# Optimization experiments

Hardware: AMD Instinct MI355X
Metric: run time of the kernel (lower is better)

## Reference

```python
import jax, jax.numpy as jnp
import numpy as np

B, S, DIN, DOUT, H = 4, 2048, 512, 512, 8
DH = DOUT // H
EPS = 1e-5


def _conv_bn(x, conv_w, conv_b, bn_gamma, bn_beta, bn_mean, bn_var):
    # x: [B, S, DIN] -> permute to [B, DIN, S] like torch
    xc = jnp.transpose(x, (0, 2, 1))
    y = jax.lax.conv_general_dilated(
        xc, conv_w, window_strides=(1,), padding=[(3, 3)],
        dimension_numbers=('NCH', 'OIH', 'NCH'))  # [B, DOUT, S]
    y = y + conv_b[None, :, None]
    # BatchNorm1d in eval mode: normalize per channel with running stats
    inv = jax.lax.rsqrt(bn_var + EPS)
    y = (y - bn_mean[None, :, None]) * (inv * bn_gamma)[None, :, None] + bn_beta[None, :, None]
    return jnp.transpose(y, (0, 2, 1))  # back to [B, S, DOUT]


def setup_inputs() -> dict:
    key = jax.random.key(0)
    ks = jax.random.split(key, 4)
    return {
        'q': jax.random.normal(ks[0], (B, S, DIN), dtype=jnp.float32),
        'k': jax.random.normal(ks[1], (B, S, DIN), dtype=jnp.float32),
        'v': jax.random.normal(ks[2], (B, S, DIN), dtype=jnp.float32),
        'conv_w': jax.random.normal(ks[3], (DOUT, DIN, 7), dtype=jnp.float32) * 0.02,
        'conv_b': jnp.zeros((DOUT,), jnp.float32),
        'bn_gamma': jnp.ones((DOUT,), jnp.float32),
        'bn_beta': jnp.zeros((DOUT,), jnp.float32),
        'bn_mean': jnp.zeros((DOUT,), jnp.float32),
        'bn_var': jnp.ones((DOUT,), jnp.float32),
        'ln_gamma': jnp.ones((DOUT,), jnp.float32),
        'ln_beta': jnp.zeros((DOUT,), jnp.float32),
    }


def reference(q, k, v, conv_w, conv_b, bn_gamma, bn_beta, bn_mean, bn_var,
              ln_gamma, ln_beta):
    # shared conv+BN preproc applied to q, k, v, then split into heads [B,S,H,DH]
    qh = _conv_bn(q, conv_w, conv_b, bn_gamma, bn_beta, bn_mean, bn_var).reshape(B, S, H, DH)
    kh = _conv_bn(k, conv_w, conv_b, bn_gamma, bn_beta, bn_mean, bn_var).reshape(B, S, H, DH)
    vh = _conv_bn(v, conv_w, conv_b, bn_gamma, bn_beta, bn_mean, bn_var).reshape(B, S, H, DH)
    # full QK^T score matrix, scaled, softmax, times V (mask is None)
    scores = jnp.einsum('bqhd,bkhd->bhqk', qh, kh) * (1.0 / np.sqrt(DH).astype(np.float32))
    probs = jax.nn.softmax(scores, axis=-1)
    out = jnp.einsum('bhqk,bkhd->bqhd', probs, vh).reshape(B, S, DOUT)
    # dropout(p=0) is identity; final LayerNorm over feature dim
    mu = jnp.mean(out, axis=-1, keepdims=True)
    var = jnp.mean(jnp.square(out - mu), axis=-1, keepdims=True)
    return (out - mu) * jax.lax.rsqrt(var + EPS) * ln_gamma + ln_beta
```

## Files before the change

### kernel.cpp

```cpp
#include <hip/hip_runtime.h>
#include <hip/hip_bf16.h>


#define B_ 4
#define S_ 2048
#define DIN_ 512
#define DOUT_ 512
#define H_ 8
#define DH_ 64
#define EPS_ 1e-5f
#define SP_ 2054

using bf16x8 = __attribute__((ext_vector_type(8))) short;
using f32x4  = __attribute__((ext_vector_type(4))) float;

__device__ __forceinline__ unsigned short f2bf(float x) {
    union { float f; unsigned u; } v; v.f = x;
    unsigned r = v.u + 0x7FFF + ((v.u >> 16) & 1);
    return (unsigned short)(r >> 16);
}

__device__ __forceinline__ unsigned cvt2(float lo, float hi) {
    unsigned r;
    asm("v_cvt_pk_bf16_f32 %0, %1, %2" : "=v"(r) : "v"(lo), "v"(hi));
    return r;
}

typedef __attribute__((address_space(1))) const unsigned int GU32;
typedef __attribute__((address_space(3))) unsigned int LU32;
__device__ __forceinline__ void gl_lds16(const void* g, void* l) {
    __builtin_amdgcn_global_load_lds((GU32*)g, (LU32*)l, 16, 0, 0);
}

__global__ void cast_x(const float* __restrict__ q, const float* __restrict__ k,
                       const float* __restrict__ v, unsigned short* __restrict__ xb) {
    int i = blockIdx.x * 256 + threadIdx.x;
    int row = i >> 6;
    int cin = (i & 63) * 8;
    int tb = row / SP_;
    int pr = row - tb * SP_;
    int tensor = tb >> 2;
    int b = tb & 3;
    unsigned short* dst = xb + (size_t)row * DIN_ + cin;
    if (pr < 3 || pr >= SP_ - 3) {
        *reinterpret_cast<uint4*>(dst) = make_uint4(0, 0, 0, 0);
    } else {
        const float* src = (tensor == 0 ? q : (tensor == 1 ? k : v)) +
                           ((size_t)b * S_ + (pr - 3)) * DIN_ + cin;
        float4 a0 = *reinterpret_cast<const float4*>(src);
        float4 a1 = *reinterpret_cast<const float4*>(src + 4);
        uint4 o;
        o.x = cvt2(a0.x, a0.y); o.y = cvt2(a0.z, a0.w);
        o.z = cvt2(a1.x, a1.y); o.w = cvt2(a1.z, a1.w);
        *reinterpret_cast<uint4*>(dst) = o;
    }
}

__global__ void prep_w(const float* __restrict__ w, const float* __restrict__ cb,
                       const float* __restrict__ gamma, const float* __restrict__ beta,
                       const float* __restrict__ mean, const float* __restrict__ var,
                       unsigned short* __restrict__ w_eff, float* __restrict__ b_eff) {
    int gid = blockIdx.x * blockDim.x + threadIdx.x;
    if (gid < DOUT_) {
        float sc = gamma[gid] * rsqrtf(var[gid] + EPS_);
        b_eff[gid] = (cb[gid] - mean[gid]) * sc + beta[gid];
    }
    int total = 7 * DOUT_ * DIN_;
    for (int i = gid; i < total; i += gridDim.x * blockDim.x) {
        int t = i / (DOUT_ * DIN_);
        int rem = i - t * (DOUT_ * DIN_);
        int co = rem >> 9;
        int ci = rem & 511;
        float sc = gamma[co] * rsqrtf(var[co] + EPS_);
        w_eff[i] = f2bf(w[(co * DIN_ + ci) * 7 + t] * sc);
    }
}

__global__ __launch_bounds__(256, 2) void conv_bn(
        const unsigned short* __restrict__ xb,
        const unsigned short* __restrict__ w_eff,
        const float* __restrict__ b_eff,
        unsigned short* __restrict__ out3) {
    __shared__ alignas(16) unsigned short As[2][192 * 32];
    __shared__ alignas(16) unsigned short Bs[3][256 * 32];

    int orig = blockIdx.x;
    int bid = (orig & 7) * 48 + (orig >> 3);
    int tensor = bid >> 7;
    int rem = bid & 127;
    int batch = rem >> 5;
    int stile = (rem >> 1) & 15;
    int cotile = rem & 1;
    int s0 = stile * 128;
    int co0 = cotile * 256;

    const unsigned short* xp = xb + (size_t)(tensor * 4 + batch) * SP_ * DIN_;
    unsigned short* out = out3 + (size_t)tensor * (B_ * S_ * DOUT_) +
                          (size_t)batch * S_ * DOUT_;

    const int tid = threadIdx.x;
    const int l = tid & 63;
    const int wv = tid >> 6;
    const int g = l >> 4;
    const int c16 = l & 15;
    const int wrow = (wv >> 1) * 64;
    const int wcol = (wv & 1) * 128;

    const int dr4 = l >> 2;
    const int sch = ((l & 3) ^ (dr4 & 3)) << 3;

#define STAGE_A(cc, buf) do {                                                   \
        _Pragma("unroll")                                                       \
        for (int j = 0; j < 3; ++j) {                                           \
            int r0 = (wv * 3 + j) * 16;                                         \
            int rs = r0 + dr4; if (rs > 133) rs = 133;                          \
            gl_lds16(xp + (size_t)(s0 + rs) * DIN_ + (cc) * 32 + sch,           \
                     &As[buf][r0 * 32]);                                        \
        }                                                                       \
    } while (0)

#define STAGE_B(cc, t, buf) do {                                                \
        const unsigned short* wp = w_eff + (size_t)(t) * (DOUT_ * DIN_) +       \
                                   (cc) * 32;                                   \
        _Pragma("unroll")                                                       \
        for (int j = 0; j < 4; ++j) {                                           \
            int r0 = (wv * 4 + j) * 16;                                         \
            gl_lds16(wp + (size_t)(co0 + r0 + dr4) * DIN_ + sch,                \
                     &Bs[buf][r0 * 32]);                                        \
        }                                                                       \
    } while (0)

    f32x4 acc[4][8] = {};

    STAGE_A(0, 0);
    STAGE_B(0, 0, 0);
    int bcur = 0;

    for (int cc = 0; cc < 16; ++cc) {
        const int ca = cc & 1;
        for (int t = 0; t < 7; ++t) {
            int bnext = bcur + 1; if (bnext == 3) bnext = 0;
            if (t < 6) {
                STAGE_B(cc, t + 1, bnext);
                asm volatile("s_waitcnt vmcnt(4)" ::: "memory");
            } else if (cc < 15) {
                STAGE_B(cc + 1, 0, bnext);
                STAGE_A(cc + 1, ca ^ 1);
                asm volatile("s_waitcnt vmcnt(7)" ::: "memory");
            } else {
                asm volatile("s_waitcnt vmcnt(0)" ::: "memory");
            }
            __builtin_amdgcn_s_barrier();

            const unsigned short* Ab = &As[ca][0];
            const unsigned short* Bb = &Bs[bcur][0];
            bf16x8 af[4], bfv[8];
#pragma unroll
            for (int m = 0; m < 4; ++m) {
                int r = wrow + m * 16 + c16 + t;
                af[m] = *reinterpret_cast<const bf16x8*>(
                    &Ab[r * 32 + ((g ^ (r & 3)) << 3)]);
            }
#pragma unroll
            for (int n = 0; n < 8; ++n) {
                int rb = wcol + n * 16 + c16;
                bfv[n] = *reinterpret_cast<const bf16x8*>(
                    &Bb[rb * 32 + ((g ^ (rb & 3)) << 3)]);
            }
            __builtin_amdgcn_s_setprio(1);
#pragma unroll
            for (int m = 0; m < 4; ++m)
#pragma unroll
                for (int n = 0; n < 8; ++n)
                    acc[m][n] = __builtin_amdgcn_mfma_f32_16x16x32_bf16(
                        af[m], bfv[n], acc[m][n], 0, 0, 0);
            __builtin_amdgcn_s_setprio(0);
            bcur = bnext;
        }
    }

    float osc = (tensor == 0) ? 0.125f : 1.0f;
#pragma unroll
    for (int m = 0; m < 4; ++m) {
        int rowb = s0 + wrow + m * 16 + 4 * g;
#pragma unroll
        for (int n = 0; n < 8; ++n) {
            int col = co0 + wcol + n * 16 + c16;
            float be = b_eff[col];
#pragma unroll
            for (int ri = 0; ri < 4; ++ri)
                out[(size_t)(rowb + ri) * DOUT_ + col] =
                    f2bf((acc[m][n][ri] + be) * osc);
        }
    }
#undef STAGE_A
#undef STAGE_B
}

__global__ void transpose_v(const unsigned short* __restrict__ vh,
                            unsigned short* __restrict__ vt) {
    __shared__ alignas(16) unsigned short T[64 * 64];
    int bid = blockIdx.x;
    int stile = bid & 31;
    int bh = bid >> 5;
    int b = bh >> 3;
    int h = bh & 7;
    int s0 = stile * 64;
    const unsigned short* src = vh + ((size_t)b * S_ + s0) * DOUT_ + h * DH_;
    unsigned short* dst = vt + (size_t)bh * DH_ * S_ + s0;
    int tid = threadIdx.x;
#pragma unroll
    for (int it = 0; it < 2; ++it) {
        int idx = tid + it * 256;
        int s = idx >> 3, dhc = idx & 7;
        uint4 val = *reinterpret_cast<const uint4*>(&src[(size_t)s * DOUT_ + dhc * 8]);
        *reinterpret_cast<uint4*>(&T[s * 64 + ((dhc ^ (s & 7) ^ ((s >> 3) & 7)) << 3)]) = val;
    }
    __syncthreads();
#pragma unroll
    for (int it = 0; it < 2; ++it) {
        int idx = tid + it * 256;
        int dh = idx >> 3, sc = idx & 7;
        unsigned short tmp[8];
#pragma unroll
        for (int j = 0; j < 8; ++j) {
            int s = sc * 8 + j;
            tmp[j] = T[s * 64 + (((dh >> 3) ^ (s & 7) ^ ((s >> 3) & 7)) << 3) + (dh & 7)];
        }
        *reinterpret_cast<uint4*>(&dst[(size_t)dh * S_ + sc * 8]) =
            *reinterpret_cast<const uint4*>(tmp);
    }
}

__global__ __launch_bounds__(256, 4) void attn(const unsigned short* __restrict__ qh,
                     const unsigned short* __restrict__ kh,
                     const unsigned short* __restrict__ vt,
                     float* __restrict__ out) {
    __shared__ alignas(16) unsigned short Ks[2][64 * 64];
    __shared__ alignas(16) unsigned short Vs[2][64 * 64];
    __shared__ alignas(16) unsigned short Ps[4][16 * 64];

    const int tid = threadIdx.x;
    const int l = tid & 63;
    const int wv = tid >> 6;
    const int g = l >> 4;
    const int c16 = l & 15;

    const int orig = blockIdx.x;
    const int bid = ((orig & 7) << 7) + (orig >> 3);
    const int qt = bid & 31;
    const int bh = bid >> 5;
    const int b = bh >> 3;
    const int h = bh & 7;
    const int s0 = qt * 64;

    const unsigned short* qp = qh + (size_t)b * S_ * DOUT_ + h * DH_;
    const unsigned short* kp = kh + (size_t)b * S_ * DOUT_ + h * DH_;
    const unsigned short* vp = vt + (size_t)bh * DH_ * S_;

    bf16x8 qf[2];
    {
        int row = s0 + wv * 16 + c16;
        qf[0] = *reinterpret_cast<const bf16x8*>(&qp[(size_t)row * DOUT_ + 8 * g]);
        qf[1] = *reinterpret_cast<const bf16x8*>(&qp[(size_t)row * DOUT_ + 32 + 8 * g]);
    }

    const int l3 = l >> 3;
    const int kchunk8 = ((l & 7) ^ l3) * 8;

#define STAGE(kt, buf) do {                                                          \
        const unsigned short* kgp = kp + (size_t)(kt) * 64 * DOUT_;                  \
        const unsigned short* vgp = vp + (size_t)(kt) * 64;                          \
        _Pragma("unroll")                                                            \
        for (int i = 0; i < 2; ++i) {                                                \
            int K0 = wv * 16 + i * 8;                                                \
            gl_lds16(kgp + (size_t)(K0 + l3) * DOUT_ + kchunk8, &Ks[buf][K0 * 64]);  \
            gl_lds16(vgp + (size_t)(K0 + l3) * S_   + kchunk8, &Vs[buf][K0 * 64]);   \
        }                                                                            \
    } while (0)

    f32x4 oacc[4] = {};
    float mrow[4], lrow[4];
#pragma unroll
    for (int r = 0; r < 4; ++r) { mrow[r] = -1e30f; lrow[r] = 0.f; }

    char* PsB = (char*)&Ps[wv][0];

    STAGE(0, 0);

    const int NT = S_ / 64;
    for (int kt = 0; kt < NT; ++kt) {
        const int cur = kt & 1;
        if (kt + 1 < NT) {
            STAGE(kt + 1, 1 - cur);
            asm volatile("s_waitcnt vmcnt(4)" ::: "memory");
        } else {
            asm volatile("s_waitcnt vmcnt(0)" ::: "memory");
        }
        __builtin_amdgcn_s_barrier();

        const char* KsB = (const char*)&Ks[cur][0];
        f32x4 sf[4] = {};
#pragma unroll
        for (int kk = 0; kk < 2; ++kk) {
            bf16x8 kf[4];
#pragma unroll
            for (int n = 0; n < 4; ++n)
                kf[n] = *reinterpret_cast<const bf16x8*>(
                    KsB + (n * 16 + c16) * 128 + (((4 * kk + g) ^ (l & 7)) << 4));
            __builtin_amdgcn_s_setprio(1);
#pragma unroll
            for (int n = 0; n < 4; ++n)
                sf[n] = __builtin_amdgcn_mfma_f32_16x16x32_bf16(qf[kk], kf[n], sf[n], 0, 0, 0);
            __builtin_amdgcn_s_setprio(0);
        }

        float mnew[4], corr[4];
#pragma unroll
        for (int r = 0; r < 4; ++r) {
            float mx = fmaxf(fmaxf(sf[0][r], sf[1][r]), fmaxf(sf[2][r], sf[3][r]));
            mx = fmaxf(mx, __shfl_xor(mx, 1, 64));
            mx = fmaxf(mx, __shfl_xor(mx, 2, 64));
            mx = fmaxf(mx, __shfl_xor(mx, 4, 64));
            mx = fmaxf(mx, __shfl_xor(mx, 8, 64));
            mnew[r] = fmaxf(mrow[r], mx);
            corr[r] = __expf(mrow[r] - mnew[r]);
            mrow[r] = mnew[r];
        }
        float rs[4] = {0.f, 0.f, 0.f, 0.f};
#pragma unroll
        for (int n = 0; n < 4; ++n)
#pragma unroll
            for (int r = 0; r < 4; ++r) {
                float p = __expf(sf[n][r] - mnew[r]);
                sf[n][r] = p;
                rs[r] += p;
            }
#pragma unroll
        for (int r = 0; r < 4; ++r) {
            rs[r] += __shfl_xor(rs[r], 1, 64);
            rs[r] += __shfl_xor(rs[r], 2, 64);
            rs[r] += __shfl_xor(rs[r], 4, 64);
            rs[r] += __shfl_xor(rs[r], 8, 64);
            lrow[r] = lrow[r] * corr[r] + rs[r];
            oacc[0][r] *= corr[r];
            oacc[1][r] *= corr[r];
            oacc[2][r] *= corr[r];
            oacc[3][r] *= corr[r];
        }

#pragma unroll
        for (int n = 0; n < 4; ++n) {
            int cb = 2 * n + (c16 >> 3);
#pragma unroll
            for (int r = 0; r < 4; ++r) {
                int row = 4 * g + r;
                int phys = cb ^ (row & 7) ^ (row >> 3);
                *(unsigned short*)(PsB + row * 128 + (phys << 4) + ((l & 7) << 1)) =
                    f2bf(sf[n][r]);
            }
        }

        const char* VsB = (const char*)&Vs[cur][0];
#pragma unroll
        for (int kk = 0; kk < 2; ++kk) {
            int physr = (4 * kk + g) ^ (c16 & 7) ^ (c16 >> 3);
            bf16x8 pf = *reinterpret_cast<const bf16x8*>(PsB + c16 * 128 + (physr << 4));
            bf16x8 vfr[4];
#pragma unroll
            for (int n = 0; n < 4; ++n)
                vfr[n] = *reinterpret_cast<const bf16x8*>(
                    VsB + (n * 16 + c16) * 128 + (((4 * kk + g) ^ (l & 7)) << 4));
            __builtin_amdgcn_s_setprio(1);
#pragma unroll
            for (int n = 0; n < 4; ++n)
                oacc[n] = __builtin_amdgcn_mfma_f32_16x16x32_bf16(pf, vfr[n], oacc[n], 0, 0, 0);
            __builtin_amdgcn_s_setprio(0);
        }
        __builtin_amdgcn_s_barrier();
    }

    float* op = out + (size_t)b * S_ * DOUT_ + h * DH_;
#pragma unroll
    for (int r = 0; r < 4; ++r) {
        int row = s0 + wv * 16 + 4 * g + r;
        float inv = 1.0f / lrow[r];
#pragma unroll
        for (int n = 0; n < 4; ++n)
            op[(size_t)row * DOUT_ + n * 16 + c16] = oacc[n][r] * inv;
    }
#undef STAGE
}

__global__ void lnorm(float* __restrict__ out, const float* __restrict__ gamma,
                      const float* __restrict__ beta) {
    int tid = threadIdx.x;
    int lane = tid & 63;
    int wv = tid >> 6;
    int row = blockIdx.x * 4 + wv;
    float* p = out + (size_t)row * DOUT_;
    float4 v0 = *reinterpret_cast<const float4*>(&p[lane * 8]);
    float4 v1 = *reinterpret_cast<const float4*>(&p[lane * 8 + 4]);
    float s = v0.x + v0.y + v0.z + v0.w + v1.x + v1.y + v1.z + v1.w;
    float sq = v0.x * v0.x + v0.y * v0.y + v0.z * v0.z + v0.w * v0.w +
               v1.x * v1.x + v1.y * v1.y + v1.z * v1.z + v1.w * v1.w;
    for (int off = 1; off < 64; off <<= 1) {
        s += __shfl_xor(s, off, 64);
        sq += __shfl_xor(sq, off, 64);
    }
    float mu = s * (1.0f / 512.0f);
    float var = sq * (1.0f / 512.0f) - mu * mu;
    float rstd = rsqrtf(fmaxf(var, 0.f) + EPS_);
    float4 g0 = *reinterpret_cast<const float4*>(&gamma[lane * 8]);
    float4 g1 = *reinterpret_cast<const float4*>(&gamma[lane * 8 + 4]);
    float4 b0 = *reinterpret_cast<const float4*>(&beta[lane * 8]);
    float4 b1 = *reinterpret_cast<const float4*>(&beta[lane * 8 + 4]);
    float4 o0, o1;
    o0.x = (v0.x - mu) * rstd * g0.x + b0.x;
    o0.y = (v0.y - mu) * rstd * g0.y + b0.y;
    o0.z = (v0.z - mu) * rstd * g0.z + b0.z;
    o0.w = (v0.w - mu) * rstd * g0.w + b0.w;
    o1.x = (v1.x - mu) * rstd * g1.x + b1.x;
    o1.y = (v1.y - mu) * rstd * g1.y + b1.y;
    o1.z = (v1.z - mu) * rstd * g1.z + b1.z;
    o1.w = (v1.w - mu) * rstd * g1.w + b1.w;
    *reinterpret_cast<float4*>(&p[lane * 8]) = o0;
    *reinterpret_cast<float4*>(&p[lane * 8 + 4]) = o1;
}

extern "C" void kernel_launch(void* const* d_in, const int* in_sizes, int n_in,
                              void* d_out, int out_size, void* d_ws, size_t ws_size,
                              hipStream_t stream) {
    const float* q        = (const float*)d_in[0];
    const float* k        = (const float*)d_in[1];
    const float* v        = (const float*)d_in[2];
    const float* conv_w   = (const float*)d_in[3];
    const float* conv_b   = (const float*)d_in[4];
    const float* bn_gamma = (const float*)d_in[5];
    const float* bn_beta  = (const float*)d_in[6];
    const float* bn_mean  = (const float*)d_in[7];
    const float* bn_var   = (const float*)d_in[8];
    const float* ln_gamma = (const float*)d_in[9];
    const float* ln_beta  = (const float*)d_in[10];

    unsigned short* qh    = (unsigned short*)d_ws;
    unsigned short* kh    = qh + (size_t)B_ * S_ * DOUT_;
    unsigned short* vh    = kh + (size_t)B_ * S_ * DOUT_;
    unsigned short* w_eff = vh + (size_t)B_ * S_ * DOUT_;
    float* b_eff          = (float*)(w_eff + (size_t)7 * DOUT_ * DIN_);
    unsigned short* xb    = (unsigned short*)(b_eff + DOUT_);
    unsigned short* vt    = xb;

    float* out = (float*)d_out;

    cast_x<<<dim3(6162), dim3(256), 0, stream>>>(q, k, v, xb);
    prep_w<<<dim3(7168), dim3(256), 0, stream>>>(conv_w, conv_b, bn_gamma, bn_beta,
                                                 bn_mean, bn_var, w_eff, b_eff);
    conv_bn<<<dim3(384), dim3(256), 0, stream>>>(xb, w_eff, b_eff, qh);
    transpose_v<<<dim3(1024), dim3(256), 0, stream>>>(vh, vt);
    attn<<<dim3(1024), dim3(256), 0, stream>>>(qh, kh, vt, out);
    lnorm<<<dim3(2048), dim3(256), 0, stream>>>(out, ln_gamma, ln_beta);
}
```

Before: 217.1 us.

## Fold log2e into Q scale, use raw exp2, and lazily rescale softmax max

Q is prescaled by log2(e) in the conv epilogue so attention can call the hardware v_exp_f32 (exp2) directly instead of __expf. The online-softmax max update and the rescaling of accumulators are skipped unless some row's new max exceeds the running max by more than 8 (in log2 units), saving exp and multiply work per tile. The block-index swizzle is removed, so blocks are scheduled in linear order. The threshold lets the unnormalized probabilities grow up to 256x, which bf16 P and fp32 accumulators tolerate, though it adds a wave-uniform branch.

New measurement: 219.0 us. Within noise of the previous version (+0.9%).

```diff
diff --git a/kernel.cpp b/kernel.cpp
--- a/kernel.cpp
+++ b/kernel.cpp
@@ -23,6 +23,12 @@
 __device__ __forceinline__ unsigned cvt2(float lo, float hi) {
     unsigned r;
     asm("v_cvt_pk_bf16_f32 %0, %1, %2" : "=v"(r) : "v"(lo), "v"(hi));
+    return r;
+}
+
+__device__ __forceinline__ float fexp2(float x) {
+    float r;
+    asm("v_exp_f32 %0, %1" : "=v"(r) : "v"(x));
     return r;
 }
 
@@ -179,7 +185,7 @@
         }
     }
 
-    float osc = (tensor == 0) ? 0.125f : 1.0f;
+    float osc = (tensor == 0) ? 0.125f * 1.44269504f : 1.0f;
 #pragma unroll
     for (int m = 0; m < 4; ++m) {
         int rowb = s0 + wrow + m * 16 + 4 * g;
@@ -246,8 +252,7 @@
     const int g = l >> 4;
     const int c16 = l & 15;
 
-    const int orig = blockIdx.x;
-    const int bid = ((orig & 7) << 7) + (orig >> 3);
+    const int bid = blockIdx.x;
     const int qt = bid & 31;
     const int bh = bid >> 5;
     const int b = bh >> 3;
@@ -315,24 +320,37 @@
             __builtin_amdgcn_s_setprio(0);
         }
 
-        float mnew[4], corr[4];
+        float mx[4];
 #pragma unroll
         for (int r = 0; r < 4; ++r) {
-            float mx = fmaxf(fmaxf(sf[0][r], sf[1][r]), fmaxf(sf[2][r], sf[3][r]));
-            mx = fmaxf(mx, __shfl_xor(mx, 1, 64));
-            mx = fmaxf(mx, __shfl_xor(mx, 2, 64));
-            mx = fmaxf(mx, __shfl_xor(mx, 4, 64));
-            mx = fmaxf(mx, __shfl_xor(mx, 8, 64));
-            mnew[r] = fmaxf(mrow[r], mx);
-            corr[r] = __expf(mrow[r] - mnew[r]);
-            mrow[r] = mnew[r];
+            float m0 = fmaxf(fmaxf(sf[0][r], sf[1][r]), fmaxf(sf[2][r], sf[3][r]));
+            m0 = fmaxf(m0, __shfl_xor(m0, 1, 64));
+            m0 = fmaxf(m0, __shfl_xor(m0, 2, 64));
+            m0 = fmaxf(m0, __shfl_xor(m0, 4, 64));
+            m0 = fmaxf(m0, __shfl_xor(m0, 8, 64));
+            mx[r] = m0;
+        }
+        bool ok = (mx[0] <= mrow[0] + 8.f) && (mx[1] <= mrow[1] + 8.f) &&
+                  (mx[2] <= mrow[2] + 8.f) && (mx[3] <= mrow[3] + 8.f);
+        if (!__all(ok)) {
+#pragma unroll
+            for (int r = 0; r < 4; ++r) {
+                float mnew = fmaxf(mrow[r], mx[r]);
+                float corr = fexp2(mrow[r] - mnew);
+                mrow[r] = mnew;
+                lrow[r] *= corr;
+                oacc[0][r] *= corr;
+                oacc[1][r] *= corr;
+                oacc[2][r] *= corr;
+                oacc[3][r] *= corr;
+            }
         }
         float rs[4] = {0.f, 0.f, 0.f, 0.f};
 #pragma unroll
         for (int n = 0; n < 4; ++n)
 #pragma unroll
             for (int r = 0; r < 4; ++r) {
-                float p = __expf(sf[n][r] - mnew[r]);
+                float p = fexp2(sf[n][r] - mrow[r]);
                 sf[n][r] = p;
                 rs[r] += p;
             }
@@ -342,11 +360,7 @@
             rs[r] += __shfl_xor(rs[r], 2, 64);
             rs[r] += __shfl_xor(rs[r], 4, 64);
             rs[r] += __shfl_xor(rs[r], 8, 64);
-            lrow[r] = lrow[r] * corr[r] + rs[r];
-            oacc[0][r] *= corr[r];
-            oacc[1][r] *= corr[r];
-            oacc[2][r] *= corr[r];
-            oacc[3][r] *= corr[r];
+            lrow[r] += rs[r];
         }
 
 #pragma unroll
```

## Transpose attention MFMAs, keep P in registers, exp2 with lazy max rescale

Applied to the files above, without the earlier changes.

Swaps the MFMA operand order so each lane holds a whole query row's scores (S^T). Row max and sum then need only two cross-lane shuffles, and P can be packed to bf16 and redistributed by shuffles instead of going through LDS. The log2(e) factor is folded into the Q projection scale so softmax can use the raw v_exp_f32. Rescaling of the accumulator is skipped unless the max grows by more than 8 (a lazy threshold). It also removes the block-index swizzle and writes the output with vector stores. The trade-offs are more shuffle and select instructions, a looser numerical bound on the un-rescaled exponent, and possible changes in L2 locality from dropping the swizzle.

After: 188.0 us. -13.4%, faster.

```diff
diff --git a/kernel.cpp b/kernel.cpp
--- a/kernel.cpp
+++ b/kernel.cpp
@@ -23,6 +23,12 @@
 __device__ __forceinline__ unsigned cvt2(float lo, float hi) {
     unsigned r;
     asm("v_cvt_pk_bf16_f32 %0, %1, %2" : "=v"(r) : "v"(lo), "v"(hi));
+    return r;
+}
+
+__device__ __forceinline__ float fexp2(float x) {
+    float r;
+    asm("v_exp_f32 %0, %1" : "=v"(r) : "v"(x));
     return r;
 }
 
@@ -179,7 +185,7 @@
         }
     }
 
-    float osc = (tensor == 0) ? 0.125f : 1.0f;
+    float osc = (tensor == 0) ? 0.125f * 1.44269504f : 1.0f;
 #pragma unroll
     for (int m = 0; m < 4; ++m) {
         int rowb = s0 + wrow + m * 16 + 4 * g;
@@ -238,7 +244,6 @@
                      float* __restrict__ out) {
     __shared__ alignas(16) unsigned short Ks[2][64 * 64];
     __shared__ alignas(16) unsigned short Vs[2][64 * 64];
-    __shared__ alignas(16) unsigned short Ps[4][16 * 64];
 
     const int tid = threadIdx.x;
     const int l = tid & 63;
@@ -246,8 +251,7 @@
     const int g = l >> 4;
     const int c16 = l & 15;
 
-    const int orig = blockIdx.x;
-    const int bid = ((orig & 7) << 7) + (orig >> 3);
+    const int bid = blockIdx.x;
     const int qt = bid & 31;
     const int bh = bid >> 5;
     const int b = bh >> 3;
@@ -280,11 +284,11 @@
     } while (0)
 
     f32x4 oacc[4] = {};
-    float mrow[4], lrow[4];
-#pragma unroll
-    for (int r = 0; r < 4; ++r) { mrow[r] = -1e30f; lrow[r] = 0.f; }
-
-    char* PsB = (char*)&Ps[wv][0];
+    float mrow = -1e30f, lrow = 0.f;
+
+    const int sA = ((l & 16) << 1) | c16;
+    const int sB = sA + 16;
+    const bool hi = (l & 32) != 0;
 
     STAGE(0, 0);
 
@@ -311,61 +315,61 @@
             __builtin_amdgcn_s_setprio(1);
 #pragma unroll
             for (int n = 0; n < 4; ++n)
-                sf[n] = __builtin_amdgcn_mfma_f32_16x16x32_bf16(qf[kk], kf[n], sf[n], 0, 0, 0);
+                sf[n] = __builtin_amdgcn_mfma_f32_16x16x32_bf16(kf[n], qf[kk], sf[n], 0, 0, 0);
             __builtin_amdgcn_s_setprio(0);
         }
 
-        float mnew[4], corr[4];
-#pragma unroll
-        for (int r = 0; r < 4; ++r) {
-            float mx = fmaxf(fmaxf(sf[0][r], sf[1][r]), fmaxf(sf[2][r], sf[3][r]));
-            mx = fmaxf(mx, __shfl_xor(mx, 1, 64));
-            mx = fmaxf(mx, __shfl_xor(mx, 2, 64));
-            mx = fmaxf(mx, __shfl_xor(mx, 4, 64));
-            mx = fmaxf(mx, __shfl_xor(mx, 8, 64));
-            mnew[r] = fmaxf(mrow[r], mx);
-            corr[r] = __expf(mrow[r] - mnew[r]);
-            mrow[r] = mnew[r];
-        }
-        float rs[4] = {0.f, 0.f, 0.f, 0.f};
-#pragma unroll
-        for (int n = 0; n < 4; ++n)
-#pragma unroll
-            for (int r = 0; r < 4; ++r) {
-                float p = __expf(sf[n][r] - mnew[r]);
-                sf[n][r] = p;
-                rs[r] += p;
+        float t0 = fmaxf(fmaxf(sf[0][0], sf[0][1]), fmaxf(sf[0][2], sf[0][3]));
+        float t1 = fmaxf(fmaxf(sf[1][0], sf[1][1]), fmaxf(sf[1][2], sf[1][3]));
+        float t2 = fmaxf(fmaxf(sf[2][0], sf[2][1]), fmaxf(sf[2][2], sf[2][3]));
+        float t3 = fmaxf(fmaxf(sf[3][0], sf[3][1]), fmaxf(sf[3][2], sf[3][3]));
+        float m0 = fmaxf(fmaxf(t0, t1), fmaxf(t2, t3));
+        m0 = fmaxf(m0, __shfl_xor(m0, 16, 64));
+        m0 = fmaxf(m0, __shfl_xor(m0, 32, 64));
+        if (!__all(m0 <= mrow + 8.f)) {
+            float mnew = fmaxf(mrow, m0);
+            float corr = fexp2(mrow - mnew);
+            mrow = mnew;
+            lrow *= corr;
+#pragma unroll
+            for (int n = 0; n < 4; ++n) {
+                oacc[n][0] *= corr; oacc[n][1] *= corr;
+                oacc[n][2] *= corr; oacc[n][3] *= corr;
             }
-#pragma unroll
-        for (int r = 0; r < 4; ++r) {
-            rs[r] += __shfl_xor(rs[r], 1, 64);
-            rs[r] += __shfl_xor(rs[r], 2, 64);
-            rs[r] += __shfl_xor(rs[r], 4, 64);
-            rs[r] += __shfl_xor(rs[r], 8, 64);
-            lrow[r] = lrow[r] * corr[r] + rs[r];
-            oacc[0][r] *= corr[r];
-            oacc[1][r] *= corr[r];
-            oacc[2][r] *= corr[r];
-            oacc[3][r] *= corr[r];
-        }
-
+        }
+        unsigned pk[4][2];
+        float rsn[4];
 #pragma unroll
         for (int n = 0; n < 4; ++n) {
-            int cb = 2 * n + (c16 >> 3);
-#pragma unroll
-            for (int r = 0; r < 4; ++r) {
-                int row = 4 * g + r;
-                int phys = cb ^ (row & 7) ^ (row >> 3);
-                *(unsigned short*)(PsB + row * 128 + (phys << 4) + ((l & 7) << 1)) =
-                    f2bf(sf[n][r]);
-            }
-        }
+            float p0 = fexp2(sf[n][0] - mrow);
+            float p1 = fexp2(sf[n][1] - mrow);
+            float p2 = fexp2(sf[n][2] - mrow);
+            float p3 = fexp2(sf[n][3] - mrow);
+            rsn[n] = (p0 + p1) + (p2 + p3);
+            pk[n][0] = cvt2(p0, p1);
+            pk[n][1] = cvt2(p2, p3);
+        }
+        float rs = (rsn[0] + rsn[1]) + (rsn[2] + rsn[3]);
+        rs += __shfl_xor(rs, 16, 64);
+        rs += __shfl_xor(rs, 32, 64);
+        lrow += rs;
 
         const char* VsB = (const char*)&Vs[cur][0];
 #pragma unroll
         for (int kk = 0; kk < 2; ++kk) {
-            int physr = (4 * kk + g) ^ (c16 & 7) ^ (c16 >> 3);
-            bf16x8 pf = *reinterpret_cast<const bf16x8*>(PsB + c16 * 128 + (physr << 4));
+            unsigned a0 = __shfl((int)pk[2 * kk][0], sA, 64);
+            unsigned a1 = __shfl((int)pk[2 * kk][1], sA, 64);
+            unsigned a2 = __shfl((int)pk[2 * kk][0], sB, 64);
+            unsigned a3 = __shfl((int)pk[2 * kk][1], sB, 64);
+            unsigned b0 = __shfl((int)pk[2 * kk + 1][0], sA, 64);
+            unsigned b1 = __shfl((int)pk[2 * kk + 1][1], sA, 64);
+            unsigned b2 = __shfl((int)pk[2 * kk + 1][0], sB, 64);
+            unsigned b3 = __shfl((int)pk[2 * kk + 1][1], sB, 64);
+            union { unsigned w[4]; bf16x8 v; } pu;
+            pu.w[0] = hi ? b0 : a0;
+            pu.w[1] = hi ? b1 : a1;
+            pu.w[2] = hi ? b2 : a2;
+            pu.w[3] = hi ? b3 : a3;
             bf16x8 vfr[4];
 #pragma unroll
             for (int n = 0; n < 4; ++n)
@@ -374,20 +378,22 @@
             __builtin_amdgcn_s_setprio(1);
 #pragma unroll
             for (int n = 0; n < 4; ++n)
-                oacc[n] = __builtin_amdgcn_mfma_f32_16x16x32_bf16(pf, vfr[n], oacc[n], 0, 0, 0);
+                oacc[n] = __builtin_amdgcn_mfma_f32_16x16x32_bf16(vfr[n], pu.v, oacc[n], 0, 0, 0);
             __builtin_amdgcn_s_setprio(0);
         }
         __builtin_amdgcn_s_barrier();
     }
 
-    float* op = out + (size_t)b * S_ * DOUT_ + h * DH_;
-#pragma unroll
-    for (int r = 0; r < 4; ++r) {
-        int row = s0 + wv * 16 + 4 * g + r;
-        float inv = 1.0f / lrow[r];
-#pragma unroll
-        for (int n = 0; n < 4; ++n)
-            op[(size_t)row * DOUT_ + n * 16 + c16] = oacc[n][r] * inv;
+    {
+        int row = s0 + wv * 16 + c16;
+        float inv = 1.0f / lrow;
+        float* op = out + (size_t)b * S_ * DOUT_ + h * DH_ + (size_t)row * DOUT_;
+#pragma unroll
+        for (int n = 0; n < 4; ++n) {
+            f32x4 o = oacc[n];
+            o[0] *= inv; o[1] *= inv; o[2] *= inv; o[3] *= inv;
+            *reinterpret_cast<f32x4*>(&op[n * 16 + 4 * g]) = o;
+        }
     }
 #undef STAGE
 }
```
